# Performance work log

Measured on AMD Instinct MI355X. Metric: run time of the kernel, lower is better.

Reference implementation:

```python
import jax, jax.numpy as jnp
import numpy as np


def setup_inputs() -> dict:
    key = jax.random.key(0)
    kx, km = jax.random.split(key)
    B, D, O = 16384, 256, 32
    x = jax.random.normal(kx, (B, D), dtype=jnp.float32)
    M = jax.random.uniform(km, (D, O), dtype=jnp.float32)
    return {"x": x, "M": M}


def reference(x, M):
    # NMU forward: y[b, o] = prod_d (M_hat[d, o] * x[b, d] + 1 - M_hat[d, o])
    M_hat = jnp.clip(M, 0.0, 1.0)                      # [D, O]
    # affine broadcast: [B, D, 1] * [1, D, O] -> [B, D, O]
    t = x[:, :, None] * M_hat[None, :, :] + (1.0 - M_hat)[None, :, :]
    return jnp.prod(t, axis=1)                          # [B, O]
```

## Files before the change

kernel.cpp:

```cpp
#include <hip/hip_runtime.h>


constexpr int D  = 256;
constexpr int O  = 32;
constexpr int SLOTS = 8;
constexpr int R  = 4;
constexpr int ROWS_PER_BLOCK = SLOTS * R;
constexpr int DC = 32;

__global__ __launch_bounds__(256) void nmu_fwd_kernel(
    const float* __restrict__ x, const float* __restrict__ M,
    float* __restrict__ y)
{
    const int o    = threadIdx.x & 31;
    const int slot = threadIdx.x >> 5;
    const int row0 = blockIdx.x * ROWS_PER_BLOCK + slot;

    float prod[R];
#pragma unroll
    for (int i = 0; i < R; ++i) prod[i] = 1.0f;

#pragma unroll
    for (int dc = 0; dc < D; dc += DC) {
        float mh[DC], om[DC];
#pragma unroll
        for (int j = 0; j < DC; ++j) {
            float v = M[(dc + j) * O + o];
            v = __builtin_amdgcn_fmed3f(v, 0.0f, 1.0f);
            mh[j] = v;
            om[j] = 1.0f - v;
        }

#pragma unroll
        for (int i = 0; i < R; ++i) {
            const int row = row0 + i * SLOTS;
            const float4* xp = reinterpret_cast<const float4*>(x + row * D + dc);
            float p = prod[i];
#pragma unroll
            for (int q = 0; q < DC / 4; ++q) {
                float4 xv = xp[q];
                float t0 = fmaf(xv.x, mh[4*q+0], om[4*q+0]);
                float t1 = fmaf(xv.y, mh[4*q+1], om[4*q+1]);
                float t2 = fmaf(xv.z, mh[4*q+2], om[4*q+2]);
                float t3 = fmaf(xv.w, mh[4*q+3], om[4*q+3]);
                p = p * ((t0 * t1) * (t2 * t3));
            }
            prod[i] = p;
        }
    }

#pragma unroll
    for (int i = 0; i < R; ++i) {
        const int row = row0 + i * SLOTS;
        y[row * O + o] = prod[i];
    }
}

extern "C" void kernel_launch(void* const* d_in, const int* in_sizes, int n_in,
                              void* d_out, int out_size, void* d_ws, size_t ws_size,
                              hipStream_t stream) {
    const float* x = (const float*)d_in[0];
    const float* M = (const float*)d_in[1];
    float* y = (float*)d_out;
    const int B = in_sizes[0] / D;
    dim3 grid(B / ROWS_PER_BLOCK);
    nmu_fwd_kernel<<<grid, 256, 0, stream>>>(x, M, y);
}
```

Measured before the change: 80.52 us.

## Stage x tiles into LDS with async double-buffered global_load_lds

Each block now copies its 32-row slice of x into a double-buffered shared-memory tile in 64-column chunks, using async global-to-LDS loads. The next chunk is prefetched while the current one is computed from LDS. Before, every lane issued its own broadcast global float4 loads of x, and this change replaces those redundant global accesses with LDS reads whose latency overlaps compute. It adds 16KB of LDS per block and a barrier per chunk, and it relies on the barrier also waiting for the async LDS writes.

```diff
diff --git a/kernel.cpp b/kernel.cpp
--- a/kernel.cpp
+++ b/kernel.cpp
@@ -1,59 +1,91 @@
 #include <hip/hip_runtime.h>
+#include <stdint.h>
 
 
-constexpr int D  = 256;
-constexpr int O  = 32;
+constexpr int D = 256;
+constexpr int O = 32;
 constexpr int SLOTS = 8;
-constexpr int R  = 4;
-constexpr int ROWS_PER_BLOCK = SLOTS * R;
-constexpr int DC = 32;
+constexpr int R = 4;
+constexpr int ROWS = SLOTS * R;
+constexpr int DC = 64;
+constexpr int NCHUNK = D / DC;
+constexpr int F4_PER_ROW = DC / 4;
+constexpr int CHUNK_F4 = ROWS * F4_PER_ROW;
 
-__global__ __launch_bounds__(256) void nmu_fwd_kernel(
-    const float* __restrict__ x, const float* __restrict__ M,
-    float* __restrict__ y)
+__device__ __forceinline__ void async16(const float* g, float* l) {
+    __builtin_amdgcn_global_load_lds(
+        (const __attribute__((address_space(1))) uint32_t*)g,
+        (__attribute__((address_space(3))) uint32_t*)l, 16, 0, 0);
+}
+
+__global__ __launch_bounds__(256) void nmu_fwd(const float* __restrict__ x,
+                                               const float* __restrict__ M,
+                                               float* __restrict__ y)
 {
-    const int o    = threadIdx.x & 31;
-    const int slot = threadIdx.x >> 5;
-    const int row0 = blockIdx.x * ROWS_PER_BLOCK + slot;
+    __shared__ float xb[2][ROWS * DC];
+    const int tid  = threadIdx.x;
+    const int o    = tid & 31;
+    const int slot = tid >> 5;
+    const int row0 = blockIdx.x * ROWS;
+
+    auto stage = [&](int k, int b) {
+#pragma unroll
+        for (int it = 0; it < CHUNK_F4 / 256; ++it) {
+            const int f = it * 256 + tid;
+            const int r = f / F4_PER_ROW;
+            const int c = f % F4_PER_ROW;
+            async16(x + (row0 + r) * D + k * DC + c * 4, &xb[b][f * 4]);
+        }
+    };
+
+    stage(0, 0);
 
     float prod[R];
 #pragma unroll
     for (int i = 0; i < R; ++i) prod[i] = 1.0f;
 
-#pragma unroll
-    for (int dc = 0; dc < D; dc += DC) {
-        float mh[DC], om[DC];
-#pragma unroll
-        for (int j = 0; j < DC; ++j) {
-            float v = M[(dc + j) * O + o];
-            v = __builtin_amdgcn_fmed3f(v, 0.0f, 1.0f);
-            mh[j] = v;
-            om[j] = 1.0f - v;
-        }
+    __syncthreads();
 
 #pragma unroll
-        for (int i = 0; i < R; ++i) {
-            const int row = row0 + i * SLOTS;
-            const float4* xp = reinterpret_cast<const float4*>(x + row * D + dc);
-            float p = prod[i];
+    for (int k = 0; k < NCHUNK; ++k) {
+        if (k + 1 < NCHUNK) stage(k + 1, (k + 1) & 1);
+        const float* buf = xb[k & 1];
+
 #pragma unroll
-            for (int q = 0; q < DC / 4; ++q) {
-                float4 xv = xp[q];
-                float t0 = fmaf(xv.x, mh[4*q+0], om[4*q+0]);
-                float t1 = fmaf(xv.y, mh[4*q+1], om[4*q+1]);
-                float t2 = fmaf(xv.z, mh[4*q+2], om[4*q+2]);
-                float t3 = fmaf(xv.w, mh[4*q+3], om[4*q+3]);
-                p = p * ((t0 * t1) * (t2 * t3));
+        for (int s = 0; s < DC / 32; ++s) {
+            float mh[32], om[32];
+            const int d0 = k * DC + s * 32;
+#pragma unroll
+            for (int j = 0; j < 32; ++j) {
+                float v = M[(d0 + j) * O + o];
+                v = __builtin_amdgcn_fmed3f(v, 0.0f, 1.0f);
+                mh[j] = v;
+                om[j] = 1.0f - v;
             }
-            prod[i] = p;
+#pragma unroll
+            for (int i = 0; i < R; ++i) {
+                const int r = slot + i * SLOTS;
+                const float4* xp =
+                    reinterpret_cast<const float4*>(buf + r * DC + s * 32);
+                float p = prod[i];
+#pragma unroll
+                for (int q = 0; q < 8; ++q) {
+                    float4 xv = xp[q];
+                    float t0 = fmaf(xv.x, mh[4*q+0], om[4*q+0]);
+                    float t1 = fmaf(xv.y, mh[4*q+1], om[4*q+1]);
+                    float t2 = fmaf(xv.z, mh[4*q+2], om[4*q+2]);
+                    float t3 = fmaf(xv.w, mh[4*q+3], om[4*q+3]);
+                    p = p * ((t0 * t1) * (t2 * t3));
+                }
+                prod[i] = p;
+            }
         }
+        __syncthreads();
     }
 
 #pragma unroll
-    for (int i = 0; i < R; ++i) {
-        const int row = row0 + i * SLOTS;
-        y[row * O + o] = prod[i];
-    }
+    for (int i = 0; i < R; ++i)
+        y[(row0 + slot + i * SLOTS) * O + o] = prod[i];
 }
 
 extern "C" void kernel_launch(void* const* d_in, const int* in_sizes, int n_in,
@@ -63,6 +95,6 @@
     const float* M = (const float*)d_in[1];
     float* y = (float*)d_out;
     const int B = in_sizes[0] / D;
-    dim3 grid(B / ROWS_PER_BLOCK);
-    nmu_fwd_kernel<<<grid, 256, 0, stream>>>(x, M, y);
+    dim3 grid(B / ROWS);
+    nmu_fwd<<<grid, 256, 0, stream>>>(x, M, y);
 }
```

New measurement: 222.4 us. 2.76x slower.

## Split reduction dimension across half-waves and use packed float2 math

Applied to the files above, without the earlier changes.

Each 64-lane wavefront is split into two halves that each reduce half of the D dimension, and the halves are combined with a cross-lane shuffle. Each wave now handles 2 rows instead of 4 per slot, and the block covers 8 rows, so the grid grows fourfold. The clamp, FMA and multiplies use 2-wide vector types so the compiler can emit packed FP32 instructions. The occupancy hint is raised and the loop is only partially unrolled to reduce register pressure. In exchange, each M value is loaded by fewer rows, so there is more M traffic per row, and half the lanes sit idle during the final store.

```diff
diff --git a/kernel.cpp b/kernel.cpp
--- a/kernel.cpp
+++ b/kernel.cpp
@@ -1,58 +1,79 @@
 #include <hip/hip_runtime.h>
 
 
-constexpr int D  = 256;
-constexpr int O  = 32;
-constexpr int SLOTS = 8;
-constexpr int R  = 4;
-constexpr int ROWS_PER_BLOCK = SLOTS * R;
-constexpr int DC = 32;
+typedef float v2f __attribute__((ext_vector_type(2)));
 
-__global__ __launch_bounds__(256) void nmu_fwd_kernel(
-    const float* __restrict__ x, const float* __restrict__ M,
-    float* __restrict__ y)
+constexpr int D    = 256;
+constexpr int O    = 32;
+constexpr int R    = 2;
+constexpr int ROWS = 4 * R;
+constexpr int HD   = D / 2;
+constexpr int DM   = 8;
+
+__global__ __launch_bounds__(256, 4) void nmu_fwd(const float* __restrict__ x,
+                                                  const float* __restrict__ M,
+                                                  float* __restrict__ y)
 {
-    const int o    = threadIdx.x & 31;
-    const int slot = threadIdx.x >> 5;
-    const int row0 = blockIdx.x * ROWS_PER_BLOCK + slot;
+    const int tid  = threadIdx.x;
+    const int o    = tid & 31;
+    const int h    = (tid >> 5) & 1;
+    const int w    = tid >> 6;
+    const int row0 = blockIdx.x * ROWS + w * R;
 
-    float prod[R];
+    const float* xr0 = x + row0 * D + h * HD;
+    const float* xr1 = xr0 + D;
+    const float* Mp  = M + (h * HD) * O + o;
+
+    v2f p0 = {1.0f, 1.0f};
+    v2f p1 = {1.0f, 1.0f};
+
+#pragma unroll 2
+    for (int c = 0; c < HD / DM; ++c) {
+        v2f mh[DM / 2], om[DM / 2];
 #pragma unroll
-    for (int i = 0; i < R; ++i) prod[i] = 1.0f;
-
-#pragma unroll
-    for (int dc = 0; dc < D; dc += DC) {
-        float mh[DC], om[DC];
-#pragma unroll
-        for (int j = 0; j < DC; ++j) {
-            float v = M[(dc + j) * O + o];
-            v = __builtin_amdgcn_fmed3f(v, 0.0f, 1.0f);
+        for (int j = 0; j < DM / 2; ++j) {
+            float a = Mp[(c * DM + 2 * j    ) * O];
+            float b = Mp[(c * DM + 2 * j + 1) * O];
+            v2f v = {a, b};
+            v = __builtin_elementwise_max(v, (v2f)0.0f);
+            v = __builtin_elementwise_min(v, (v2f)1.0f);
             mh[j] = v;
-            om[j] = 1.0f - v;
+            om[j] = (v2f)1.0f - v;
         }
 
-#pragma unroll
-        for (int i = 0; i < R; ++i) {
-            const int row = row0 + i * SLOTS;
-            const float4* xp = reinterpret_cast<const float4*>(x + row * D + dc);
-            float p = prod[i];
-#pragma unroll
-            for (int q = 0; q < DC / 4; ++q) {
-                float4 xv = xp[q];
-                float t0 = fmaf(xv.x, mh[4*q+0], om[4*q+0]);
-                float t1 = fmaf(xv.y, mh[4*q+1], om[4*q+1]);
-                float t2 = fmaf(xv.z, mh[4*q+2], om[4*q+2]);
-                float t3 = fmaf(xv.w, mh[4*q+3], om[4*q+3]);
-                p = p * ((t0 * t1) * (t2 * t3));
-            }
-            prod[i] = p;
+        const float4* xp0 = reinterpret_cast<const float4*>(xr0 + c * DM);
+        const float4* xp1 = reinterpret_cast<const float4*>(xr1 + c * DM);
+        float4 A0 = xp0[0], B0 = xp0[1];
+        float4 A1 = xp1[0], B1 = xp1[1];
+
+        {
+            v2f t0 = {A0.x, A0.y}, t1 = {A0.z, A0.w};
+            v2f t2 = {B0.x, B0.y}, t3 = {B0.z, B0.w};
+            t0 = __builtin_elementwise_fma(t0, mh[0], om[0]);
+            t1 = __builtin_elementwise_fma(t1, mh[1], om[1]);
+            t2 = __builtin_elementwise_fma(t2, mh[2], om[2]);
+            t3 = __builtin_elementwise_fma(t3, mh[3], om[3]);
+            p0 *= (t0 * t1) * (t2 * t3);
+        }
+        {
+            v2f t0 = {A1.x, A1.y}, t1 = {A1.z, A1.w};
+            v2f t2 = {B1.x, B1.y}, t3 = {B1.z, B1.w};
+            t0 = __builtin_elementwise_fma(t0, mh[0], om[0]);
+            t1 = __builtin_elementwise_fma(t1, mh[1], om[1]);
+            t2 = __builtin_elementwise_fma(t2, mh[2], om[2]);
+            t3 = __builtin_elementwise_fma(t3, mh[3], om[3]);
+            p1 *= (t0 * t1) * (t2 * t3);
         }
     }
 
-#pragma unroll
-    for (int i = 0; i < R; ++i) {
-        const int row = row0 + i * SLOTS;
-        y[row * O + o] = prod[i];
+    float q0 = p0.x * p0.y;
+    float q1 = p1.x * p1.y;
+    q0 *= __shfl_xor(q0, 32, 64);
+    q1 *= __shfl_xor(q1, 32, 64);
+
+    if (h == 0) {
+        y[(row0    ) * O + o] = q0;
+        y[(row0 + 1) * O + o] = q1;
     }
 }
 
@@ -63,6 +84,6 @@
     const float* M = (const float*)d_in[1];
     float* y = (float*)d_out;
     const int B = in_sizes[0] / D;
-    dim3 grid(B / ROWS_PER_BLOCK);
-    nmu_fwd_kernel<<<grid, 256, 0, stream>>>(x, M, y);
+    dim3 grid(B / ROWS);
+    nmu_fwd<<<grid, 256, 0, stream>>>(x, M, y);
 }
```

New measurement: 84.12 us. +4.5%, slower.

## Keep clamped M slice in registers, split D across half-waves, packed FMA with prefetch

Applied to the files above, without the earlier changes.

Each 64-lane wave now splits the D reduction in two: each half-wave holds its 128 clamped M values for one output column in registers for the whole block. It then walks 8 rows sequentially, rewriting the term as m*(x-1)+1 so packed two-wide float math can be used. x loads are double-buffered in chunks of 8 float4, and the two half-products are combined with a cross-lane shuffle. This removes the repeated M reloads and the 1-m computation per chunk. In exchange it raises register pressure (128 M values plus 64 buffered x floats) and launches the same grid size with fewer independent rows in flight per thread.

```diff
diff --git a/kernel.cpp b/kernel.cpp
--- a/kernel.cpp
+++ b/kernel.cpp
@@ -1,58 +1,77 @@
 #include <hip/hip_runtime.h>
 
 
+typedef float v2f __attribute__((ext_vector_type(2)));
+
 constexpr int D  = 256;
 constexpr int O  = 32;
-constexpr int SLOTS = 8;
-constexpr int R  = 4;
-constexpr int ROWS_PER_BLOCK = SLOTS * R;
-constexpr int DC = 32;
+constexpr int HD = D / 2;
+constexpr int ROWS_PW = 8;
+constexpr int WAVES   = 4;
+constexpr int ROWS_PB = ROWS_PW * WAVES;
 
-__global__ __launch_bounds__(256) void nmu_fwd_kernel(
-    const float* __restrict__ x, const float* __restrict__ M,
-    float* __restrict__ y)
+__global__ __launch_bounds__(256, 2)
+void nmu_fwd(const float* __restrict__ x, const float* __restrict__ M,
+             float* __restrict__ y)
 {
-    const int o    = threadIdx.x & 31;
-    const int slot = threadIdx.x >> 5;
-    const int row0 = blockIdx.x * ROWS_PER_BLOCK + slot;
+    const int tid  = threadIdx.x;
+    const int lane = tid & 63;
+    const int w    = tid >> 6;
+    const int o    = lane & 31;
+    const int dh   = lane >> 5;
+    const int row0 = blockIdx.x * ROWS_PB + w * ROWS_PW;
 
-    float prod[R];
+    v2f m[HD / 2];
+    const float* Mp = M + (dh * HD) * O + o;
 #pragma unroll
-    for (int i = 0; i < R; ++i) prod[i] = 1.0f;
+    for (int j = 0; j < HD / 2; ++j) {
+        float a = Mp[(2 * j    ) * O];
+        float b = Mp[(2 * j + 1) * O];
+        m[j].x = __builtin_amdgcn_fmed3f(a, 0.0f, 1.0f);
+        m[j].y = __builtin_amdgcn_fmed3f(b, 0.0f, 1.0f);
+    }
 
+    const float* xbase = x + dh * HD;
+
+#pragma unroll 1
+    for (int r = 0; r < ROWS_PW; ++r) {
+        const int row = row0 + r;
+        const float4* xp = reinterpret_cast<const float4*>(xbase + row * D);
+
+        float4 cur[8], nxt[8];
 #pragma unroll
-    for (int dc = 0; dc < D; dc += DC) {
-        float mh[DC], om[DC];
+        for (int u = 0; u < 8; ++u) cur[u] = xp[u];
+
+        v2f p = {1.0f, 1.0f};
 #pragma unroll
-        for (int j = 0; j < DC; ++j) {
-            float v = M[(dc + j) * O + o];
-            v = __builtin_amdgcn_fmed3f(v, 0.0f, 1.0f);
-            mh[j] = v;
-            om[j] = 1.0f - v;
+        for (int c = 0; c < 4; ++c) {
+            if (c < 3) {
+#pragma unroll
+                for (int u = 0; u < 8; ++u) nxt[u] = xp[(c + 1) * 8 + u];
+            }
+            v2f t[16];
+#pragma unroll
+            for (int u = 0; u < 8; ++u) {
+                const int f = c * 8 + u;
+                v2f x01 = {cur[u].x - 1.0f, cur[u].y - 1.0f};
+                v2f x23 = {cur[u].z - 1.0f, cur[u].w - 1.0f};
+                t[2 * u]     = m[2 * f]     * x01 + (v2f){1.0f, 1.0f};
+                t[2 * u + 1] = m[2 * f + 1] * x23 + (v2f){1.0f, 1.0f};
+            }
+#pragma unroll
+            for (int i = 0; i < 8; ++i) t[i] *= t[i + 8];
+#pragma unroll
+            for (int i = 0; i < 4; ++i) t[i] *= t[i + 4];
+            t[0] *= t[2]; t[1] *= t[3];
+            p *= t[0] * t[1];
+#pragma unroll
+            for (int u = 0; u < 8; ++u) cur[u] = nxt[u];
         }
 
-#pragma unroll
-        for (int i = 0; i < R; ++i) {
-            const int row = row0 + i * SLOTS;
-            const float4* xp = reinterpret_cast<const float4*>(x + row * D + dc);
-            float p = prod[i];
-#pragma unroll
-            for (int q = 0; q < DC / 4; ++q) {
-                float4 xv = xp[q];
-                float t0 = fmaf(xv.x, mh[4*q+0], om[4*q+0]);
-                float t1 = fmaf(xv.y, mh[4*q+1], om[4*q+1]);
-                float t2 = fmaf(xv.z, mh[4*q+2], om[4*q+2]);
-                float t3 = fmaf(xv.w, mh[4*q+3], om[4*q+3]);
-                p = p * ((t0 * t1) * (t2 * t3));
-            }
-            prod[i] = p;
-        }
-    }
-
-#pragma unroll
-    for (int i = 0; i < R; ++i) {
-        const int row = row0 + i * SLOTS;
-        y[row * O + o] = prod[i];
+        float s = p.x * p.y;
+        s *= __shfl_xor(s, 32, 64);
+        if (dh == 0)
+            y[row * O + o] = s;
     }
 }
 
@@ -63,6 +82,6 @@
     const float* M = (const float*)d_in[1];
     float* y = (float*)d_out;
     const int B = in_sizes[0] / D;
-    dim3 grid(B / ROWS_PER_BLOCK);
-    nmu_fwd_kernel<<<grid, 256, 0, stream>>>(x, M, y);
+    dim3 grid(B / ROWS_PB);
+    nmu_fwd<<<grid, 256, 0, stream>>>(x, M, y);
 }
```

Measured after the change: 80.39 us. Within noise of the previous version (-0.2%).
